# Kernel tuning notes

Hardware: AMD Instinct MI355X
Metric: run time of the kernel (lower is better)

## Reference

```python
import jax, jax.numpy as jnp
import numpy as np

N_SPK, M_UTT, D_EMB = 8192, 10, 128
CLAMP_MIN = 1e-6


def setup_inputs() -> dict:
    key = jax.random.key(0)
    x = jax.random.normal(key, (N_SPK, M_UTT, D_EMB), dtype=jnp.float32)
    w = jnp.asarray(10.0, dtype=jnp.float32)   # learned scale (init_w)
    b = jnp.asarray(-5.0, dtype=jnp.float32)   # learned bias  (init_b)
    return {"x": x, "w": w, "b": b}


def reference(x, w, b):
    # x: [N, M, D]. Faithful to the torch module:
    #   - centroids = mean over all M utterances per speaker
    #   - calc_new_centroids replaces speaker's own centroid with mean(dvecs[spkr,:M]),
    #     which IS the full centroid -> new_centroids == centroids (no-op, kept faithful)
    #   - only the last utterance (utt_indx == M-1) contributes a row -> [N, 1, N]
    n, m, d = x.shape
    centroids = jnp.mean(x, axis=1)                       # [N, D]
    last = x[:, m - 1, :]                                 # [N, D] last utterance per speaker
    num = jnp.einsum('nd,kd->nk', last, centroids)        # [N, N]
    denom = (jnp.linalg.norm(last, axis=1)[:, None]
             * jnp.linalg.norm(centroids, axis=1)[None, :])
    cos_sim = jnp.clip(num / denom, CLAMP_MIN)            # torch.clamp(x, 1e-6) = min-clamp
    logits = cos_sim * w + b                              # [N, N] (view(-1, N) with M=1)
    # CrossEntropyLoss with labels arange(N) (repeat_interleave with M=1 is identity)
    logp = jax.nn.log_softmax(logits, axis=-1)
    labels = jnp.arange(n)
    loss = -jnp.mean(jnp.take_along_axis(logp, labels[:, None], axis=1))
    return loss
```

## Files before the change

kernel.cpp:

```cpp
#include <hip/hip_runtime.h>
#include <hip/hip_bf16.h>


typedef __attribute__((ext_vector_type(8))) short short8;
typedef __attribute__((ext_vector_type(4))) float f32x4;

#define NSPK 8192
#define DEMB 128
#define MUTT 10

#define WS_SPART 64
#define WS_ZDIAG 32832
#define WS_LASTB 262144
#define WS_CENTB 2359296

__global__ void k1_prep(const float* __restrict__ x,
                        float* __restrict__ W,
                        __hip_bfloat16* __restrict__ lastb,
                        __hip_bfloat16* __restrict__ centb) {
    const int n = blockIdx.x;
    const int d = threadIdx.x;
    const float* xr = x + (size_t)n * (MUTT * DEMB);
    float s = 0.f, v = 0.f;
#pragma unroll
    for (int m = 0; m < MUTT; ++m) { v = xr[m * DEMB + d]; s += v; }
    const float c = s * 0.1f;
    const float lastv = v;
    float sc = c * c, sl = lastv * lastv;
#pragma unroll
    for (int off = 1; off < 64; off <<= 1) {
        sc += __shfl_xor(sc, off);
        sl += __shfl_xor(sl, off);
    }
    __shared__ float red[4];
    const int wv = d >> 6;
    if ((d & 63) == 0) { red[wv * 2] = sc; red[wv * 2 + 1] = sl; }
    __syncthreads();
    sc = red[0] + red[2];
    sl = red[1] + red[3];
    const float ic = rsqrtf(sc), il = rsqrtf(sl);
    lastb[n * DEMB + d] = __float2bfloat16(lastv * il);
    centb[n * DEMB + d] = __float2bfloat16(c * ic);
    if (n == 0 && d == 0) W[0] = 0.f;
}

__global__ __launch_bounds__(256, 2) void k2_main(
        const __hip_bfloat16* __restrict__ lastb,
        const __hip_bfloat16* __restrict__ centb,
        const float* __restrict__ wp,
        float* __restrict__ W) {
    const int tid  = threadIdx.x;
    const int lane = tid & 63;
    const int wv   = tid >> 6;
    const int quad = lane >> 4;
    const int l16  = lane & 15;
    const int R0   = blockIdx.x * 64;
    const int C0   = blockIdx.y * 2048;
    const float wlog2e = wp[0] * 1.44269504088896340736f;
    const float zmin   = 1e-6f * wlog2e;

    __shared__ __hip_bfloat16 Bs[64 * 136];

    short8 a[4];
    {
        const short* ap = (const short*)(lastb + (size_t)(R0 + wv * 16 + l16) * DEMB + quad * 8);
#pragma unroll
        for (int kc = 0; kc < 4; ++kc) a[kc] = *(const short8*)(ap + kc * 32);
    }

    const int myrow0 = R0 + wv * 16 + quad * 4;
    float racc[4] = {0.f, 0.f, 0.f, 0.f};

    for (int it = 0; it < 32; ++it) {
        const int c0 = C0 + it * 64;
        __syncthreads();
        {
            const uint4* src = (const uint4*)(centb + (size_t)c0 * DEMB);
#pragma unroll
            for (int i = 0; i < 4; ++i) {
                const int idx = tid + i * 256;
                const int row = idx >> 4, ch = idx & 15;
                *((uint4*)&Bs[row * 136 + ch * 8]) = src[row * 16 + ch];
            }
        }
        __syncthreads();
#pragma unroll
        for (int nt = 0; nt < 4; ++nt) {
            f32x4 acc = {0.f, 0.f, 0.f, 0.f};
            const short* bp = (const short*)&Bs[(nt * 16 + l16) * 136 + quad * 8];
#pragma unroll
            for (int kc = 0; kc < 4; ++kc) {
                short8 b = *(const short8*)(bp + kc * 32);
                acc = __builtin_amdgcn_mfma_f32_16x16x32_bf16(a[kc], b, acc, 0, 0, 0);
            }
            const int col = c0 + nt * 16 + l16;
#pragma unroll
            for (int r = 0; r < 4; ++r) {
                const float z = fmaxf(acc[r] * wlog2e, zmin);
                racc[r] += exp2f(z);
                if (col == myrow0 + r) W[WS_ZDIAG + col] = z;
            }
        }
    }
#pragma unroll
    for (int off = 1; off < 16; off <<= 1) {
#pragma unroll
        for (int r = 0; r < 4; ++r) racc[r] += __shfl_xor(racc[r], off);
    }
    if (l16 == 0) {
#pragma unroll
        for (int r = 0; r < 4; ++r)
            W[WS_SPART + blockIdx.y * NSPK + myrow0 + r] = racc[r];
    }
}

__global__ void k3_loss(float* __restrict__ W) {
    const int n = blockIdx.x * 256 + threadIdx.x;
    const float P = W[WS_SPART + n] + W[WS_SPART + NSPK + n] +
                    W[WS_SPART + 2 * NSPK + n] + W[WS_SPART + 3 * NSPK + n];
    float v = __log2f(P) - W[WS_ZDIAG + n];
#pragma unroll
    for (int off = 1; off < 64; off <<= 1) v += __shfl_xor(v, off);
    __shared__ float red[4];
    if ((threadIdx.x & 63) == 0) red[threadIdx.x >> 6] = v;
    __syncthreads();
    if (threadIdx.x == 0) atomicAdd(&W[0], red[0] + red[1] + red[2] + red[3]);
}

__global__ void k4_fin(const float* __restrict__ W, float* __restrict__ out) {
    out[0] = W[0] * (0.69314718055994530942f / (float)NSPK);
}

extern "C" void kernel_launch(void* const* d_in, const int* in_sizes, int n_in,
                              void* d_out, int out_size, void* d_ws, size_t ws_size,
                              hipStream_t stream) {
    const float* x = (const float*)d_in[0];
    const float* w = (const float*)d_in[1];
    float* W = (float*)d_ws;
    __hip_bfloat16* lastb = (__hip_bfloat16*)((char*)d_ws + WS_LASTB);
    __hip_bfloat16* centb = (__hip_bfloat16*)((char*)d_ws + WS_CENTB);

    k1_prep<<<NSPK, DEMB, 0, stream>>>(x, W, lastb, centb);
    k2_main<<<dim3(128, 4), 256, 0, stream>>>(lastb, centb, w, W);
    k3_loss<<<NSPK / 256, 256, 0, stream>>>(W);
    k4_fin<<<1, 1, 0, stream>>>(W, (float*)d_out);
}
```

Before: 131.3 us.

## Retile similarity GEMM, fold scale into A, compute diagonal in prep, merge kernels

The prep kernel now handles one speaker per wave with float2 loads. It pre-multiplies the normalized last-utterance vectors by w*log2e and computes the diagonal logit directly as a dot product. The main kernel uses 256x512 block tiles with each wave holding a 64-row A tile in registers, loads B through swizzled global_load_lds, and accumulates row sums with atomics into a zeroed buffer. The loss and finalize kernels are merged into a single-block reduction. Together these aim to cut B-tile reloads, per-element multiplies and diagonal checks, and launch count, at the cost of atomics, more register pressure, and a serial single-block reduction.

```diff
diff --git a/kernel.cpp b/kernel.cpp
--- a/kernel.cpp
+++ b/kernel.cpp
@@ -8,40 +8,54 @@
 #define NSPK 8192
 #define DEMB 128
 #define MUTT 10
+#define LOG2E 1.44269504088896340736f
+#define LN2   0.69314718055994530942f
 
-#define WS_SPART 64
-#define WS_ZDIAG 32832
-#define WS_LASTB 262144
-#define WS_CENTB 2359296
+#define WS_ZDIAG 0
+#define WS_ZSUM  8192
+#define WS_LASTB 65536
+#define WS_CENTB 2162688
 
-__global__ void k1_prep(const float* __restrict__ x,
-                        float* __restrict__ W,
-                        __hip_bfloat16* __restrict__ lastb,
-                        __hip_bfloat16* __restrict__ centb) {
-    const int n = blockIdx.x;
-    const int d = threadIdx.x;
-    const float* xr = x + (size_t)n * (MUTT * DEMB);
-    float s = 0.f, v = 0.f;
+__global__ __launch_bounds__(256) void k1_prep(const float* __restrict__ x,
+                                               const float* __restrict__ wp,
+                                               float* __restrict__ W,
+                                               __hip_bfloat16* __restrict__ lastb,
+                                               __hip_bfloat16* __restrict__ centb) {
+    const int wv = threadIdx.x >> 6;
+    const int l  = threadIdx.x & 63;
+    const int n  = blockIdx.x * 4 + wv;
+    if (blockIdx.x < 32) W[WS_ZSUM + blockIdx.x * 256 + threadIdx.x] = 0.f;
+
+    const float* xr = x + (size_t)n * (MUTT * DEMB) + 2 * l;
+    float sx = 0.f, sy = 0.f, vx = 0.f, vy = 0.f;
 #pragma unroll
-    for (int m = 0; m < MUTT; ++m) { v = xr[m * DEMB + d]; s += v; }
-    const float c = s * 0.1f;
-    const float lastv = v;
-    float sc = c * c, sl = lastv * lastv;
+    for (int m = 0; m < MUTT; ++m) {
+        float2 t = *(const float2*)(xr + m * DEMB);
+        vx = t.x; vy = t.y; sx += t.x; sy += t.y;
+    }
+    const float cx = sx * 0.1f, cy = sy * 0.1f;
+    float sl = vx * vx + vy * vy;
+    float sc = cx * cx + cy * cy;
+    float dp = vx * cx + vy * cy;
 #pragma unroll
     for (int off = 1; off < 64; off <<= 1) {
+        sl += __shfl_xor(sl, off);
         sc += __shfl_xor(sc, off);
-        sl += __shfl_xor(sl, off);
+        dp += __shfl_xor(dp, off);
     }
-    __shared__ float red[4];
-    const int wv = d >> 6;
-    if ((d & 63) == 0) { red[wv * 2] = sc; red[wv * 2 + 1] = sl; }
-    __syncthreads();
-    sc = red[0] + red[2];
-    sl = red[1] + red[3];
-    const float ic = rsqrtf(sc), il = rsqrtf(sl);
-    lastb[n * DEMB + d] = __float2bfloat16(lastv * il);
-    centb[n * DEMB + d] = __float2bfloat16(c * ic);
-    if (n == 0 && d == 0) W[0] = 0.f;
+    const float il = rsqrtf(sl), ic = rsqrtf(sc);
+    const float scale = wp[0] * LOG2E;
+    const float as = il * scale;
+    __hip_bfloat162 lv, cv;
+    lv.x = __float2bfloat16(vx * as); lv.y = __float2bfloat16(vy * as);
+    cv.x = __float2bfloat16(cx * ic); cv.y = __float2bfloat16(cy * ic);
+    *(__hip_bfloat162*)(lastb + n * DEMB + 2 * l) = lv;
+    *(__hip_bfloat162*)(centb + n * DEMB + 2 * l) = cv;
+    if (l == 0) {
+        const float lo = scale >= 0.f ? 1e-6f * scale : -INFINITY;
+        const float hi = scale >= 0.f ? INFINITY : 1e-6f * scale;
+        W[WS_ZDIAG + n] = fminf(fmaxf(dp * il * ic * scale, lo), hi);
+    }
 }
 
 __global__ __launch_bounds__(256, 2) void k2_main(
@@ -54,81 +68,96 @@
     const int wv   = tid >> 6;
     const int quad = lane >> 4;
     const int l16  = lane & 15;
-    const int R0   = blockIdx.x * 64;
-    const int C0   = blockIdx.y * 2048;
-    const float wlog2e = wp[0] * 1.44269504088896340736f;
-    const float zmin   = 1e-6f * wlog2e;
+    const int R0   = blockIdx.x * 256;
+    const int C0   = blockIdx.y * 512;
+    const float scale = wp[0] * LOG2E;
+    const float lo = scale >= 0.f ? 1e-6f * scale : -INFINITY;
+    const float hi = scale >= 0.f ? INFINITY : 1e-6f * scale;
 
-    __shared__ __hip_bfloat16 Bs[64 * 136];
+    __shared__ uint4 Bs4[1024];
+    char* Bsc = (char*)Bs4;
 
-    short8 a[4];
+    short8 a[4][4];
     {
-        const short* ap = (const short*)(lastb + (size_t)(R0 + wv * 16 + l16) * DEMB + quad * 8);
+        const short* ap = (const short*)lastb + (size_t)(R0 + wv * 64 + l16) * DEMB + quad * 8;
 #pragma unroll
-        for (int kc = 0; kc < 4; ++kc) a[kc] = *(const short8*)(ap + kc * 32);
+        for (int rt = 0; rt < 4; ++rt)
+#pragma unroll
+            for (int kc = 0; kc < 4; ++kc)
+                a[rt][kc] = *(const short8*)(ap + rt * 16 * DEMB + kc * 32);
     }
 
-    const int myrow0 = R0 + wv * 16 + quad * 4;
-    float racc[4] = {0.f, 0.f, 0.f, 0.f};
+    int roff[4];
+#pragma unroll
+    for (int kc = 0; kc < 4; ++kc)
+        roff[kc] = l16 * 256 + (((quad + 4 * kc) ^ l16) << 4);
 
-    for (int it = 0; it < 32; ++it) {
+    const int srow = wv * 16 + (lane >> 4);
+    const int sp   = lane & 15;
+    float racc[4][4] = {{0.f}};
+
+    for (int it = 0; it < 8; ++it) {
         const int c0 = C0 + it * 64;
         __syncthreads();
-        {
-            const uint4* src = (const uint4*)(centb + (size_t)c0 * DEMB);
 #pragma unroll
-            for (int i = 0; i < 4; ++i) {
-                const int idx = tid + i * 256;
-                const int row = idx >> 4, ch = idx & 15;
-                *((uint4*)&Bs[row * 136 + ch * 8]) = src[row * 16 + ch];
-            }
+        for (int i = 0; i < 4; ++i) {
+            const int row = srow + i * 4;
+            const int c   = sp ^ (row & 15);
+            const char* src = (const char*)centb + ((size_t)(c0 + row) << 8) + (c << 4);
+            char* dst = Bsc + (wv * 4096 + i * 1024 + lane * 16);
+            __builtin_amdgcn_global_load_lds(
+                (const __attribute__((address_space(1))) unsigned int*)src,
+                (__attribute__((address_space(3))) unsigned int*)dst, 16, 0, 0);
         }
         __syncthreads();
 #pragma unroll
         for (int nt = 0; nt < 4; ++nt) {
-            f32x4 acc = {0.f, 0.f, 0.f, 0.f};
-            const short* bp = (const short*)&Bs[(nt * 16 + l16) * 136 + quad * 8];
+            short8 b[4];
 #pragma unroll
-            for (int kc = 0; kc < 4; ++kc) {
-                short8 b = *(const short8*)(bp + kc * 32);
-                acc = __builtin_amdgcn_mfma_f32_16x16x32_bf16(a[kc], b, acc, 0, 0, 0);
-            }
-            const int col = c0 + nt * 16 + l16;
+            for (int kc = 0; kc < 4; ++kc)
+                b[kc] = *(const short8*)(Bsc + nt * 4096 + roff[kc]);
 #pragma unroll
-            for (int r = 0; r < 4; ++r) {
-                const float z = fmaxf(acc[r] * wlog2e, zmin);
-                racc[r] += exp2f(z);
-                if (col == myrow0 + r) W[WS_ZDIAG + col] = z;
+            for (int rt = 0; rt < 4; ++rt) {
+                f32x4 acc = {0.f, 0.f, 0.f, 0.f};
+#pragma unroll
+                for (int kc = 0; kc < 4; ++kc)
+                    acc = __builtin_amdgcn_mfma_f32_16x16x32_bf16(a[rt][kc], b[kc], acc, 0, 0, 0);
+#pragma unroll
+                for (int r = 0; r < 4; ++r) {
+                    const float z = fminf(fmaxf(acc[r], lo), hi);
+                    racc[rt][r] += exp2f(z);
+                }
             }
         }
     }
 #pragma unroll
-    for (int off = 1; off < 16; off <<= 1) {
+    for (int off = 1; off < 16; off <<= 1)
 #pragma unroll
-        for (int r = 0; r < 4; ++r) racc[r] += __shfl_xor(racc[r], off);
-    }
+        for (int rt = 0; rt < 4; ++rt)
+#pragma unroll
+            for (int r = 0; r < 4; ++r)
+                racc[rt][r] += __shfl_xor(racc[rt][r], off);
     if (l16 == 0) {
 #pragma unroll
-        for (int r = 0; r < 4; ++r)
-            W[WS_SPART + blockIdx.y * NSPK + myrow0 + r] = racc[r];
+        for (int rt = 0; rt < 4; ++rt)
+#pragma unroll
+            for (int r = 0; r < 4; ++r)
+                atomicAdd(&W[WS_ZSUM + R0 + wv * 64 + rt * 16 + quad * 4 + r], racc[rt][r]);
     }
 }
 
-__global__ void k3_loss(float* __restrict__ W) {
-    const int n = blockIdx.x * 256 + threadIdx.x;
-    const float P = W[WS_SPART + n] + W[WS_SPART + NSPK + n] +
-                    W[WS_SPART + 2 * NSPK + n] + W[WS_SPART + 3 * NSPK + n];
-    float v = __log2f(P) - W[WS_ZDIAG + n];
+__global__ __launch_bounds__(256) void k3_loss(const float* __restrict__ W,
+                                               float* __restrict__ out) {
+    float v = 0.f;
+    for (int n = threadIdx.x; n < NSPK; n += 256)
+        v += __log2f(W[WS_ZSUM + n]) - W[WS_ZDIAG + n];
 #pragma unroll
     for (int off = 1; off < 64; off <<= 1) v += __shfl_xor(v, off);
     __shared__ float red[4];
     if ((threadIdx.x & 63) == 0) red[threadIdx.x >> 6] = v;
     __syncthreads();
-    if (threadIdx.x == 0) atomicAdd(&W[0], red[0] + red[1] + red[2] + red[3]);
-}
-
-__global__ void k4_fin(const float* __restrict__ W, float* __restrict__ out) {
-    out[0] = W[0] * (0.69314718055994530942f / (float)NSPK);
+    if (threadIdx.x == 0)
+        out[0] = (red[0] + red[1] + red[2] + red[3]) * (LN2 / (float)NSPK);
 }
 
 extern "C" void kernel_launch(void* const* d_in, const int* in_sizes, int n_in,
@@ -140,8 +169,7 @@
     __hip_bfloat16* lastb = (__hip_bfloat16*)((char*)d_ws + WS_LASTB);
     __hip_bfloat16* centb = (__hip_bfloat16*)((char*)d_ws + WS_CENTB);
 
-    k1_prep<<<NSPK, DEMB, 0, stream>>>(x, W, lastb, centb);
-    k2_main<<<dim3(128, 4), 256, 0, stream>>>(lastb, centb, w, W);
-    k3_loss<<<NSPK / 256, 256, 0, stream>>>(W);
-    k4_fin<<<1, 1, 0, stream>>>(W, (float*)d_out);
+    k1_prep<<<NSPK / 4, 256, 0, stream>>>(x, w, W, lastb, centb);
+    k2_main<<<dim3(32, 16), 256, 0, stream>>>(lastb, centb, w, W);
+    k3_loss<<<1, 256, 0, stream>>>(W, (float*)d_out);
 }
```

Result: faster. 123.2 us (-6.1%).
